# Performance work log

Hardware: AMD Instinct MI355X
Metric: run time of the kernel (lower is better)

## Reference

```python
import jax, jax.numpy as jnp
import numpy as np

NUM_HEADS = 12
EMBED_DIM = 768
HEAD_DIM = EMBED_DIM // NUM_HEADS


def _rope_cos_sin():
    # Faithful to source: RoPE is applied with seq_dim=1 on [b,h,n,d] tensors,
    # so the "position" axis is actually the HEAD axis (length NUM_HEADS).
    inv_freq = 1.0 / (10000.0 ** (jnp.arange(0, HEAD_DIM, 2, dtype=jnp.float32) / HEAD_DIM))
    t = jnp.arange(NUM_HEADS, dtype=jnp.float32)
    freqs = t[:, None] * inv_freq[None, :]            # [H, D/2]
    emb = jnp.concatenate([freqs, freqs], axis=-1)     # [H, D]
    cos = jnp.cos(emb)[None, :, None, :]               # [1, H, 1, D] broadcasts over seq
    sin = jnp.sin(emb)[None, :, None, :]
    return cos, sin


def _apply_rope(x, cos, sin):
    # x: [B, H, N, D]
    x1, x2 = jnp.split(x, 2, axis=-1)
    x_rot = jnp.concatenate([-x2, x1], axis=-1)
    return x * cos + x_rot * sin


def setup_inputs() -> dict:
    key = jax.random.key(0)
    k1, k2, k3, k4, k5 = jax.random.split(key, 5)
    B, N, E = 8, 1024, EMBED_DIM
    s_in = 1.0 / np.sqrt(E)
    return {
        "x": jax.random.normal(k1, (B, N, E), dtype=jnp.float32),
        "w_qkv": jax.random.uniform(k2, (E, 3 * E), dtype=jnp.float32, minval=-s_in, maxval=s_in),
        "b_qkv": jax.random.uniform(k3, (3 * E,), dtype=jnp.float32, minval=-s_in, maxval=s_in),
        "w_proj": jax.random.uniform(k4, (E, E), dtype=jnp.float32, minval=-s_in, maxval=s_in),
        "b_proj": jax.random.uniform(k5, (E,), dtype=jnp.float32, minval=-s_in, maxval=s_in),
    }


def reference(x, w_qkv, b_qkv, w_proj, b_proj):
    B, N, E = x.shape
    H, D = NUM_HEADS, HEAD_DIM
    scale = D ** (-0.5)

    qkv = x @ w_qkv + b_qkv                                  # [B, N, 3E]
    qkv = qkv.reshape(B, N, 3, H, D).transpose(2, 0, 3, 1, 4)  # [3, B, H, N, D]
    q, k, v = qkv[0], qkv[1], qkv[2]

    cos, sin = _rope_cos_sin()
    q = _apply_rope(q, cos, sin)
    k = _apply_rope(k, cos, sin)

    attn = jnp.einsum('bhid,bhjd->bhij', q, k) * scale       # [B, H, N, N]
    attn = jax.nn.softmax(attn, axis=-1)
    out = jnp.einsum('bhij,bhjd->bhid', attn, v)             # [B, H, N, D]
    out = out.transpose(0, 2, 1, 3).reshape(B, N, E)         # [B, N, E]
    return out @ w_proj + b_proj
```

## Files before the change

### kernel.cpp

```cpp
#include <hip/hip_runtime.h>
#include <math.h>

#define NH 12
#define HD 64
#define NSEQ 1024
#define BATCH 8
#define EMB 768
#define NQKV 2304
#define MROWS 8192

typedef _Float16 half8 __attribute__((ext_vector_type(8)));
typedef _Float16 half4 __attribute__((ext_vector_type(4)));
typedef _Float16 half2v __attribute__((ext_vector_type(2)));
typedef __fp16 fp16x2 __attribute__((ext_vector_type(2)));
typedef float f32x4 __attribute__((ext_vector_type(4)));
typedef float f32x16 __attribute__((ext_vector_type(16)));
typedef unsigned int u32;

#define MFMA16(a,b,c) __builtin_amdgcn_mfma_f32_16x16x32_f16(a, b, c, 0, 0, 0)
#define MFMA32(a,b,c) __builtin_amdgcn_mfma_f32_32x32x16_f16(a, b, c, 0, 0, 0)

#define QSCALE 0.18033688011112043f
#define EXPB 5.770780163555856f

#define ASYNC16(g, l)                                                          \
  __builtin_amdgcn_global_load_lds(                                            \
      (const __attribute__((address_space(1))) unsigned int*)(g),              \
      (__attribute__((address_space(3))) unsigned int*)(l), 16, 0, 0)

__device__ __forceinline__ void transpose_tile(const float* __restrict__ in,
                                               _Float16* __restrict__ out,
                                               int R, int C, int bx, int by,
                                               _Float16 (*T)[72]) {
  const int tr = by * 64, tc = bx * 64;
  const int r = threadIdx.x >> 2, s = threadIdx.x & 3;
  const float* src = in + (size_t)(tr + r) * C + tc + s * 16;
  _Float16* dst = &T[r][s * 16];
  #pragma unroll
  for (int i = 0; i < 4; ++i) {
    float4 v = ((const float4*)src)[i];
    dst[4*i+0] = (_Float16)v.x; dst[4*i+1] = (_Float16)v.y;
    dst[4*i+2] = (_Float16)v.z; dst[4*i+3] = (_Float16)v.w;
  }
  __syncthreads();
  alignas(16) _Float16 tmp[16];
  #pragma unroll
  for (int j = 0; j < 16; ++j) tmp[j] = T[s * 16 + j][r];
  half8* o = (half8*)(out + (size_t)(tc + r) * R + tr + s * 16);
  o[0] = *(half8*)&tmp[0];
  o[1] = *(half8*)&tmp[8];
}

__global__ __launch_bounds__(256) void prepass(const float* __restrict__ x,
                                               _Float16* __restrict__ xh,
                                               const float* __restrict__ wq,
                                               _Float16* __restrict__ wqT,
                                               const float* __restrict__ wp,
                                               _Float16* __restrict__ wpT) {
  __shared__ _Float16 T[64][72];
  const int bid = blockIdx.x;
  if (bid < 6144) {
    int i = bid * 256 + threadIdx.x;
    float4 v = ((const float4*)x)[i];
    half4 h = { (_Float16)v.x, (_Float16)v.y, (_Float16)v.z, (_Float16)v.w };
    ((half4*)xh)[i] = h;
  } else if (bid < 6576) {
    int idx = bid - 6144;
    transpose_tile(wq, wqT, EMB, NQKV, idx % 36, idx / 36, T);
  } else {
    int idx = bid - 6576;
    transpose_tile(wp, wpT, EMB, EMB, idx % 12, idx / 12, T);
  }
}

__device__ __forceinline__ int xcd_remap() {
  const int flat = blockIdx.y * gridDim.x + blockIdx.x;
  const int q = (gridDim.x * gridDim.y) >> 3;
  return (flat & 7) * q + (flat >> 3);
}

__global__ __launch_bounds__(256) void gemm_qkv(const _Float16* __restrict__ A,
                                                const _Float16* __restrict__ BT,
                                                const float* __restrict__ bias,
                                                _Float16* __restrict__ qo,
                                                _Float16* __restrict__ ko,
                                                _Float16* __restrict__ vo,
                                                int K) {
  const int BUFH = 128 * 32;
  __shared__ __align__(16) _Float16 As[2 * 128 * 32];
  __shared__ __align__(16) _Float16 Bs[2 * 128 * 32];
  const int tid = threadIdx.x;
  const int lane = tid & 63, wave = tid >> 6;
  const int quad = lane >> 4, l15 = lane & 15;
  const int wm = (wave >> 1) * 64, wn = (wave & 1) * 64;
  const int nf = xcd_remap();
  const int row0 = (nf / gridDim.x) * 128, col0 = (nf % gridDim.x) * 128;

  const int srow = lane >> 2;
  const int sseg = (lane & 3) ^ ((srow >> 1) & 3);
  const _Float16* gA = A + (size_t)(row0 + wave*32 + srow) * K + sseg * 8;
  const _Float16* gB = BT + (size_t)(col0 + wave*32 + srow) * K + sseg * 8;
  _Float16* lA = As + (wave * 32) * 32;
  _Float16* lB = Bs + (wave * 32) * 32;

  const int xq = (quad ^ ((l15 >> 1) & 3)) * 8;

  f32x4 acc[4][4];
  #pragma unroll
  for (int i = 0; i < 4; ++i)
    #pragma unroll
    for (int j = 0; j < 4; ++j) {
      f32x4 z = {0.f, 0.f, 0.f, 0.f};
      acc[i][j] = z;
    }

  ASYNC16(gA,          lA);
  ASYNC16(gA + 16 * K, lA + 16*32);
  ASYNC16(gB,          lB);
  ASYNC16(gB + 16 * K, lB + 16*32);
  __syncthreads();

  int buf = 0;
  for (int k0 = 0; k0 < K; k0 += 32) {
    if (k0 + 32 < K) {
      const int nb = (buf ^ 1) * BUFH;
      ASYNC16(gA + k0 + 32,          lA + nb);
      ASYNC16(gA + k0 + 32 + 16 * K, lA + nb + 16*32);
      ASYNC16(gB + k0 + 32,          lB + nb);
      ASYNC16(gB + k0 + 32 + 16 * K, lB + nb + 16*32);
    }
    const _Float16* Ab = As + buf * BUFH;
    const _Float16* Bb = Bs + buf * BUFH;
    half8 af[4], bf[4];
    #pragma unroll
    for (int mt = 0; mt < 4; ++mt)
      af[mt] = *(const half8*)(Ab + (wm + mt*16 + l15) * 32 + xq);
    #pragma unroll
    for (int nt = 0; nt < 4; ++nt)
      bf[nt] = *(const half8*)(Bb + (wn + nt*16 + l15) * 32 + xq);
    #pragma unroll
    for (int mt = 0; mt < 4; ++mt)
      #pragma unroll
      for (int nt = 0; nt < 4; ++nt)
        acc[mt][nt] = MFMA16(af[mt], bf[nt], acc[mt][nt]);
    __syncthreads();
    buf ^= 1;
  }

  float bcol[4];
  #pragma unroll
  for (int nt = 0; nt < 4; ++nt)
    bcol[nt] = bias[col0 + wn + nt*16 + l15];

  const int ch = col0 + wn;
  const int tt = ch / EMB;
  const int hh = (ch % EMB) >> 6;
  float cs[2], sn[2];
  if (tt < 2) {
    #pragma unroll
    for (int j = 0; j < 2; ++j) {
      float fi = (float)(j*16 + l15);
      float ang = (float)hh * expf(-0.28782313662425574f * fi);
      sincosf(ang, &sn[j], &cs[j]);
    }
  }
  #pragma unroll
  for (int mt = 0; mt < 4; ++mt) {
    int m0 = row0 + wm + mt*16 + quad*4;
    int b = m0 >> 10, n0 = m0 & 1023;
    size_t bh = (size_t)(b * NH + hh);
    if (tt == 2) {
      int np = (n0 & ~12) | ((n0 & 4) << 1) | ((n0 & 8) >> 1);
      #pragma unroll
      for (int nt = 0; nt < 4; ++nt) {
        int d = nt*16 + l15;
        half4 pk;
        #pragma unroll
        for (int r = 0; r < 4; ++r)
          pk[r] = (_Float16)(acc[mt][nt][r] + bcol[nt]);
        *(half4*)(vo + (bh * HD + d) * NSEQ + np) = pk;
      }
    } else {
      _Float16* dst = (tt == 0) ? qo : ko;
      const float sc = (tt == 0) ? QSCALE : 1.0f;
      #pragma unroll
      for (int j = 0; j < 2; ++j) {
        #pragma unroll
        for (int r = 0; r < 4; ++r) {
          float lo = acc[mt][j][r]     + bcol[j];
          float hi = acc[mt][j + 2][r] + bcol[j + 2];
          float nlo = (lo * cs[j] - hi * sn[j]) * sc;
          float nhi = (hi * cs[j] + lo * sn[j]) * sc;
          size_t rowoff = (bh * NSEQ + (size_t)(n0 + r)) * HD;
          dst[rowoff + j*16 + l15]      = (_Float16)nlo;
          dst[rowoff + j*16 + l15 + 32] = (_Float16)nhi;
        }
      }
    }
  }
}

__global__ __launch_bounds__(256) void gemm_proj(const _Float16* __restrict__ A,
                                                 const _Float16* __restrict__ BT,
                                                 const float* __restrict__ bias,
                                                 float* __restrict__ outf,
                                                 int K) {
  const int ABUF = 128 * 64, BBUF = 64 * 64;
  __shared__ __align__(16) _Float16 As[2 * ABUF];
  __shared__ __align__(16) _Float16 Bs[2 * BBUF];
  const int tid = threadIdx.x;
  const int lane = tid & 63, wave = tid >> 6;
  const int quad = lane >> 4, l15 = lane & 15;
  const int wm = (wave >> 1) * 64, wn = (wave & 1) * 32;
  const int nf = xcd_remap();
  const int row0 = (nf / gridDim.x) * 128, col0 = (nf % gridDim.x) * 64;

  const int srow = lane >> 3;
  const int sseg = (lane & 7) ^ (srow & 7);
  const _Float16* gA = A  + (size_t)(row0 + wave*32 + srow) * K + sseg * 8;
  const _Float16* gB = BT + (size_t)(col0 + wave*16 + srow) * K + sseg * 8;
  _Float16* lA = As + (wave * 32) * 64;
  _Float16* lB = Bs + (wave * 16) * 64;

  f32x4 acc[4][2];
  #pragma unroll
  for (int i = 0; i < 4; ++i)
    #pragma unroll
    for (int j = 0; j < 2; ++j) {
      f32x4 z = {0.f, 0.f, 0.f, 0.f};
      acc[i][j] = z;
    }

  ASYNC16(gA,          lA);
  ASYNC16(gA +  8 * K, lA +  8*64);
  ASYNC16(gA + 16 * K, lA + 16*64);
  ASYNC16(gA + 24 * K, lA + 24*64);
  ASYNC16(gB,          lB);
  ASYNC16(gB +  8 * K, lB +  8*64);
  __syncthreads();

  int buf = 0;
  for (int k0 = 0; k0 < K; k0 += 64) {
    if (k0 + 64 < K) {
      const int na = (buf ^ 1) * ABUF, nb = (buf ^ 1) * BBUF;
      ASYNC16(gA + k0 + 64,          lA + na);
      ASYNC16(gA + k0 + 64 +  8 * K, lA + na +  8*64);
      ASYNC16(gA + k0 + 64 + 16 * K, lA + na + 16*64);
      ASYNC16(gA + k0 + 64 + 24 * K, lA + na + 24*64);
      ASYNC16(gB + k0 + 64,          lB + nb);
      ASYNC16(gB + k0 + 64 +  8 * K, lB + nb +  8*64);
    }
    const _Float16* Ab = As + buf * ABUF;
    const _Float16* Bb = Bs + buf * BBUF;
    #pragma unroll
    for (int kk = 0; kk < 2; ++kk) {
      const int x = ((kk*4 + quad) ^ (l15 & 7)) * 8;
      half8 af[4], bf[2];
      #pragma unroll
      for (int mt = 0; mt < 4; ++mt)
        af[mt] = *(const half8*)(Ab + (wm + mt*16 + l15) * 64 + x);
      #pragma unroll
      for (int nt = 0; nt < 2; ++nt)
        bf[nt] = *(const half8*)(Bb + (wn + nt*16 + l15) * 64 + x);
      #pragma unroll
      for (int mt = 0; mt < 4; ++mt)
        #pragma unroll
        for (int nt = 0; nt < 2; ++nt)
          acc[mt][nt] = MFMA16(af[mt], bf[nt], acc[mt][nt]);
    }
    __syncthreads();
    buf ^= 1;
  }

  float bcol[2];
  #pragma unroll
  for (int nt = 0; nt < 2; ++nt)
    bcol[nt] = bias[col0 + wn + nt*16 + l15];
  #pragma unroll
  for (int mt = 0; mt < 4; ++mt) {
    int m0 = row0 + wm + mt*16 + quad*4;
    #pragma unroll
    for (int nt = 0; nt < 2; ++nt)
      #pragma unroll
      for (int r = 0; r < 4; ++r)
        outf[(size_t)(m0 + r) * EMB + col0 + wn + nt*16 + l15] =
            acc[mt][nt][r] + bcol[nt];
  }
}

__global__ __launch_bounds__(256) void attn_mfma32(const _Float16* __restrict__ q,
                                                   const _Float16* __restrict__ k,
                                                   const _Float16* __restrict__ vt,
                                                   _Float16* __restrict__ ao) {
  const int BUFH = 64 * 64;
  __shared__ __align__(16) _Float16 Ks[2 * 64 * 64];
  __shared__ __align__(16) _Float16 Vs[2 * 64 * 64];
  const int tid = threadIdx.x;
  const int lane = tid & 63, wave = tid >> 6;
  const int l31 = lane & 31, hi = lane >> 5;
  const int nf = xcd_remap();
  const int bh = nf >> 3;
  const int qrow = (nf & 7) * 128 + wave * 32 + l31;
  const size_t base = (size_t)bh * NSEQ * HD;

  const _Float16* qp = q + base + (size_t)qrow * HD + hi * 8;
  half8 qf[4];
  #pragma unroll
  for (int kh = 0; kh < 4; ++kh)
    qf[kh] = *(const half8*)(qp + kh * 16);

  const int srow8 = lane >> 3;
  const int sseg8 = lane & 7;
  const int wseg8 = sseg8 ^ (srow8 & 7);
  const _Float16* kg = k + base + (size_t)(wave*16 + srow8) * HD + wseg8 * 8;
  const _Float16* vg = vt + (size_t)bh * HD * NSEQ
                       + (size_t)(wave*16 + srow8) * NSEQ + wseg8 * 8;
  _Float16* uK = Ks + (wave * 16) * 64;
  _Float16* uV = Vs + (wave * 16) * 64;

  int xofs[4];
  #pragma unroll
  for (int kh = 0; kh < 4; ++kh)
    xofs[kh] = ((kh*2 + hi) ^ (l31 & 7)) * 8;

  f32x16 O[2];
  #pragma unroll
  for (int dt = 0; dt < 2; ++dt)
    #pragma unroll
    for (int r = 0; r < 16; ++r) O[dt][r] = 0.f;
  float l = 0.f;

  ASYNC16(kg,              uK);
  ASYNC16(kg + 8 * HD,     uK + 8*64);
  ASYNC16(vg,              uV);
  ASYNC16(vg + 8 * NSEQ,   uV + 8*64);
  __syncthreads();

  int buf = 0;
  for (int c0 = 0; c0 < NSEQ; c0 += 64) {
    if (c0 + 64 < NSEQ) {
      const int nb = (buf ^ 1) * BUFH;
      const _Float16* kc = kg + (size_t)(c0 + 64) * HD;
      ASYNC16(kc,                  uK + nb);
      ASYNC16(kc + 8 * HD,         uK + nb + 8*64);
      ASYNC16(vg + c0 + 64,        uV + nb);
      ASYNC16(vg + 8*NSEQ + c0 + 64, uV + nb + 8*64);
    }
    const _Float16* Kb = Ks + buf * BUFH;
    const _Float16* Vb = Vs + buf * BUFH;

    f32x16 ct[2];
    __builtin_amdgcn_s_setprio(1);
    #pragma unroll
    for (int kt = 0; kt < 2; ++kt) {
      #pragma unroll
      for (int r = 0; r < 16; ++r) ct[kt][r] = 0.f;
      #pragma unroll
      for (int kh = 0; kh < 4; ++kh) {
        half8 kf = *(const half8*)(Kb + (kt*32 + l31) * 64 + xofs[kh]);
        ct[kt] = MFMA32(kf, qf[kh], ct[kt]);
      }
    }
    __builtin_amdgcn_s_setprio(0);

    union { half2v v; fp16x2 f; int i; } ph2[16];
    float rs0 = 0.f, rs1 = 0.f;
    #pragma unroll
    for (int rp = 0; rp < 8; ++rp) {
      float a0 = __builtin_amdgcn_exp2f(ct[0][2*rp]     - EXPB);
      float a1 = __builtin_amdgcn_exp2f(ct[0][2*rp + 1] - EXPB);
      float b0 = __builtin_amdgcn_exp2f(ct[1][2*rp]     - EXPB);
      float b1 = __builtin_amdgcn_exp2f(ct[1][2*rp + 1] - EXPB);
      rs0 += a0 + a1;
      rs1 += b0 + b1;
      ph2[rp].f     = __builtin_amdgcn_cvt_pkrtz(a0, a1);
      ph2[8 + rp].f = __builtin_amdgcn_cvt_pkrtz(b0, b1);
    }
    l += rs0 + rs1;

    __builtin_amdgcn_s_setprio(1);
    #pragma unroll
    for (int kh = 0; kh < 4; ++kh) {
      const int kt = kh >> 1;
      const int iA = kt*8 + (kh & 1)*4;
      union { half8 h; int d[4]; } pf;
      pf.d[0] = ph2[iA].i;     pf.d[1] = ph2[iA + 1].i;
      pf.d[2] = ph2[iA + 2].i; pf.d[3] = ph2[iA + 3].i;
      #pragma unroll
      for (int dt = 0; dt < 2; ++dt) {
        half8 vf = *(const half8*)(Vb + (dt*32 + l31) * 64 + xofs[kh]);
        O[dt] = MFMA32(vf, pf.h, O[dt]);
      }
    }
    __builtin_amdgcn_s_setprio(0);

    __syncthreads();
    buf ^= 1;
  }

  l += __shfl_xor(l, 32);

  const int b = bh / NH, hh = bh % NH;
  const float inv = 1.0f / l;
  _Float16* orow = ao + (size_t)(b * NSEQ + qrow) * EMB + hh * HD;
  #pragma unroll
  for (int dt = 0; dt < 2; ++dt)
    #pragma unroll
    for (int t = 0; t < 4; ++t) {
      int d0 = dt*32 + 8*t + 4*hi;
      half4 o4;
      #pragma unroll
      for (int j = 0; j < 4; ++j)
        o4[j] = (_Float16)(O[dt][4*t + j] * inv);
      *(half4*)(orow + d0) = o4;
    }
}

extern "C" void kernel_launch(void* const* d_in, const int* in_sizes, int n_in,
                              void* d_out, int out_size, void* d_ws, size_t ws_size,
                              hipStream_t stream) {
  const float* x      = (const float*)d_in[0];
  const float* w_qkv  = (const float*)d_in[1];
  const float* b_qkv  = (const float*)d_in[2];
  const float* w_proj = (const float*)d_in[3];
  const float* b_proj = (const float*)d_in[4];
  float* out = (float*)d_out;

  _Float16* xh  = (_Float16*)d_ws;
  _Float16* wqT = xh  + (size_t)MROWS * EMB;
  _Float16* wpT = wqT + (size_t)NQKV * EMB;
  _Float16* qh  = wpT + (size_t)EMB * EMB;
  _Float16* kh  = qh  + (size_t)BATCH*NH*NSEQ*HD;
  _Float16* vth = kh  + (size_t)BATCH*NH*NSEQ*HD;
  _Float16* aoh = vth + (size_t)BATCH*NH*NSEQ*HD;

  prepass<<<6720, 256, 0, stream>>>(x, xh, w_qkv, wqT, w_proj, wpT);

  gemm_qkv<<<dim3(NQKV/128, MROWS/128), 256, 0, stream>>>(
      xh, wqT, b_qkv, qh, kh, vth, EMB);

  attn_mfma32<<<dim3(NSEQ/128, BATCH*NH), 256, 0, stream>>>(qh, kh, vth, aoh);

  gemm_proj<<<dim3(EMB/64, MROWS/128), 256, 0, stream>>>(
      aoh, wpT, b_proj, out, EMB);
}
```

Measured before the change: 188.1 us.

## Software-pipeline attention: triple-buffer K/V and overlap next QK^T with softmax-PV

Replaces the double-buffered attention loop with a three-stage LDS ring buffer. The QK^T MFMAs for chunk c+1 are issued before the softmax and PV of chunk c, using two ping-pong score registers. The goal is to overlap exp/convert work with MFMA and keep async loads further ahead. In exchange it uses 50% more shared memory and more registers for the second score accumulator, which could reduce occupancy.

```diff
diff --git a/kernel.cpp b/kernel.cpp
--- a/kernel.cpp
+++ b/kernel.cpp
@@ -293,8 +293,8 @@
                                                    const _Float16* __restrict__ vt,
                                                    _Float16* __restrict__ ao) {
   const int BUFH = 64 * 64;
-  __shared__ __align__(16) _Float16 Ks[2 * 64 * 64];
-  __shared__ __align__(16) _Float16 Vs[2 * 64 * 64];
+  __shared__ __align__(16) _Float16 Ks[3 * BUFH];
+  __shared__ __align__(16) _Float16 Vs[3 * BUFH];
   const int tid = threadIdx.x;
   const int lane = tid & 63, wave = tid >> 6;
   const int l31 = lane & 31, hi = lane >> 5;
@@ -330,73 +330,85 @@
     for (int r = 0; r < 16; ++r) O[dt][r] = 0.f;
   float l = 0.f;
 
-  ASYNC16(kg,              uK);
-  ASYNC16(kg + 8 * HD,     uK + 8*64);
-  ASYNC16(vg,              uV);
-  ASYNC16(vg + 8 * NSEQ,   uV + 8*64);
+#define STAGE(c, b)                                                            \
+  { const _Float16* kc_ = kg + (size_t)((c) * 64) * HD;                        \
+    const int nb_ = (b) * BUFH;                                                \
+    ASYNC16(kc_,                    uK + nb_);                                 \
+    ASYNC16(kc_ + 8 * HD,           uK + nb_ + 8*64);                          \
+    ASYNC16(vg + (c) * 64,          uV + nb_);                                 \
+    ASYNC16(vg + 8*NSEQ + (c) * 64, uV + nb_ + 8*64); }
+
+#define QKT(b, ct)                                                             \
+  { const _Float16* Kb_ = Ks + (b) * BUFH;                                     \
+    __builtin_amdgcn_s_setprio(1);                                             \
+    _Pragma("unroll")                                                          \
+    for (int kt = 0; kt < 2; ++kt) {                                           \
+      _Pragma("unroll")                                                        \
+      for (int r = 0; r < 16; ++r) ct[kt][r] = 0.f;                            \
+      _Pragma("unroll")                                                        \
+      for (int kh = 0; kh < 4; ++kh) {                                         \
+        half8 kf = *(const half8*)(Kb_ + (kt*32 + l31) * 64 + xofs[kh]);       \
+        ct[kt] = MFMA32(kf, qf[kh], ct[kt]);                                   \
+      }                                                                        \
+    }                                                                          \
+    __builtin_amdgcn_s_setprio(0); }
+
+#define SMPV(b, ct)                                                            \
+  { union { half2v v; fp16x2 f; int i; } ph2[16];                              \
+    float rs0 = 0.f, rs1 = 0.f;                                                \
+    _Pragma("unroll")                                                          \
+    for (int rp = 0; rp < 8; ++rp) {                                           \
+      float a0 = __builtin_amdgcn_exp2f(ct[0][2*rp]     - EXPB);               \
+      float a1 = __builtin_amdgcn_exp2f(ct[0][2*rp + 1] - EXPB);               \
+      float b0 = __builtin_amdgcn_exp2f(ct[1][2*rp]     - EXPB);               \
+      float b1 = __builtin_amdgcn_exp2f(ct[1][2*rp + 1] - EXPB);               \
+      rs0 += a0 + a1;                                                          \
+      rs1 += b0 + b1;                                                          \
+      ph2[rp].f     = __builtin_amdgcn_cvt_pkrtz(a0, a1);                      \
+      ph2[8 + rp].f = __builtin_amdgcn_cvt_pkrtz(b0, b1);                      \
+    }                                                                          \
+    l += rs0 + rs1;                                                            \
+    const _Float16* Vb_ = Vs + (b) * BUFH;                                     \
+    __builtin_amdgcn_s_setprio(1);                                             \
+    _Pragma("unroll")                                                          \
+    for (int kh = 0; kh < 4; ++kh) {                                           \
+      const int kt_ = kh >> 1;                                                 \
+      const int iA_ = kt_*8 + (kh & 1)*4;                                      \
+      union { half8 h; int d[4]; } pf;                                         \
+      pf.d[0] = ph2[iA_].i;     pf.d[1] = ph2[iA_ + 1].i;                      \
+      pf.d[2] = ph2[iA_ + 2].i; pf.d[3] = ph2[iA_ + 3].i;                      \
+      _Pragma("unroll")                                                        \
+      for (int dt = 0; dt < 2; ++dt) {                                         \
+        half8 vf = *(const half8*)(Vb_ + (dt*32 + l31) * 64 + xofs[kh]);       \
+        O[dt] = MFMA32(vf, pf.h, O[dt]);                                       \
+      }                                                                        \
+    }                                                                          \
+    __builtin_amdgcn_s_setprio(0); }
+
+  f32x16 ctA[2], ctB[2];
+  const int NC = NSEQ / 64;
+
+  STAGE(0, 0);
   __syncthreads();
-
-  int buf = 0;
-  for (int c0 = 0; c0 < NSEQ; c0 += 64) {
-    if (c0 + 64 < NSEQ) {
-      const int nb = (buf ^ 1) * BUFH;
-      const _Float16* kc = kg + (size_t)(c0 + 64) * HD;
-      ASYNC16(kc,                  uK + nb);
-      ASYNC16(kc + 8 * HD,         uK + nb + 8*64);
-      ASYNC16(vg + c0 + 64,        uV + nb);
-      ASYNC16(vg + 8*NSEQ + c0 + 64, uV + nb + 8*64);
-    }
-    const _Float16* Kb = Ks + buf * BUFH;
-    const _Float16* Vb = Vs + buf * BUFH;
-
-    f32x16 ct[2];
-    __builtin_amdgcn_s_setprio(1);
-    #pragma unroll
-    for (int kt = 0; kt < 2; ++kt) {
-      #pragma unroll
-      for (int r = 0; r < 16; ++r) ct[kt][r] = 0.f;
-      #pragma unroll
-      for (int kh = 0; kh < 4; ++kh) {
-        half8 kf = *(const half8*)(Kb + (kt*32 + l31) * 64 + xofs[kh]);
-        ct[kt] = MFMA32(kf, qf[kh], ct[kt]);
-      }
-    }
-    __builtin_amdgcn_s_setprio(0);
-
-    union { half2v v; fp16x2 f; int i; } ph2[16];
-    float rs0 = 0.f, rs1 = 0.f;
-    #pragma unroll
-    for (int rp = 0; rp < 8; ++rp) {
-      float a0 = __builtin_amdgcn_exp2f(ct[0][2*rp]     - EXPB);
-      float a1 = __builtin_amdgcn_exp2f(ct[0][2*rp + 1] - EXPB);
-      float b0 = __builtin_amdgcn_exp2f(ct[1][2*rp]     - EXPB);
-      float b1 = __builtin_amdgcn_exp2f(ct[1][2*rp + 1] - EXPB);
-      rs0 += a0 + a1;
-      rs1 += b0 + b1;
-      ph2[rp].f     = __builtin_amdgcn_cvt_pkrtz(a0, a1);
-      ph2[8 + rp].f = __builtin_amdgcn_cvt_pkrtz(b0, b1);
-    }
-    l += rs0 + rs1;
-
-    __builtin_amdgcn_s_setprio(1);
-    #pragma unroll
-    for (int kh = 0; kh < 4; ++kh) {
-      const int kt = kh >> 1;
-      const int iA = kt*8 + (kh & 1)*4;
-      union { half8 h; int d[4]; } pf;
-      pf.d[0] = ph2[iA].i;     pf.d[1] = ph2[iA + 1].i;
-      pf.d[2] = ph2[iA + 2].i; pf.d[3] = ph2[iA + 3].i;
-      #pragma unroll
-      for (int dt = 0; dt < 2; ++dt) {
-        half8 vf = *(const half8*)(Vb + (dt*32 + l31) * 64 + xofs[kh]);
-        O[dt] = MFMA32(vf, pf.h, O[dt]);
-      }
-    }
-    __builtin_amdgcn_s_setprio(0);
-
+  STAGE(1, 1);
+  QKT(0, ctA);
+
+  for (int c = 0; c < NC; c += 2) {
     __syncthreads();
-    buf ^= 1;
-  }
+    if (c + 1 < NC) QKT((c + 1) % 3, ctB);
+    if (c + 2 < NC) STAGE(c + 2, (c + 2) % 3);
+    SMPV(c % 3, ctA);
+    if (c + 1 < NC) {
+      __syncthreads();
+      if (c + 2 < NC) QKT((c + 2) % 3, ctA);
+      if (c + 3 < NC) STAGE(c + 3, (c + 3) % 3);
+      SMPV((c + 1) % 3, ctB);
+    }
+  }
+
+#undef STAGE
+#undef QKT
+#undef SMPV
 
   l += __shfl_xor(l, 32);
 
```

Measured after the change: 195.5 us. +3.9%, slower.
